# Kernel optimization log

Hardware: AMD Instinct MI355X
Metric: run time of the kernel (lower is better)

The kernel has to match this reference:

```python
import jax, jax.numpy as jnp
import numpy as np

jax.config.update("jax_enable_x64", True)

MANT_SCALE = 8388608.0  # 2**23


def _decode_fp32_bits(bits):
    """[..., 32] {0,1} pulses (MSB-first IEEE-754 float32) -> float64 value."""
    f64 = jnp.float64
    sign = 1.0 - 2.0 * bits[..., 0].astype(f64)
    e = jnp.einsum('...j,j->...', bits[..., 1:9].astype(f64),
                   jnp.exp2(jnp.arange(7, -1, -1, dtype=f64)))
    frac = jnp.einsum('...j,j->...', bits[..., 9:32].astype(f64),
                      jnp.exp2(-jnp.arange(1, 24, dtype=f64)))
    normal = sign * jnp.exp2(e - 127.0) * (1.0 + frac)
    subnorm = sign * jnp.exp2(-126.0) * frac
    return jnp.where(e > 0, normal, subnorm)


def _encode_fp32_bits(y):
    """float64 value already on the fp32 grid -> [..., 32] {0,1} pulses (MSB-first)."""
    f64 = jnp.float64
    sbit = (y < 0).astype(f64)
    a = jnp.abs(y)
    e = jnp.clip(jnp.floor(jnp.log2(jnp.where(a > 0, a, 1.0))), -126.0, 127.0)
    eb = jnp.where(a > 0, e + 127.0, 0.0)          # biased exponent, 0 for zero/subnormal
    frac = jnp.where(eb > 0, a * jnp.exp2(-e) - 1.0, a * jnp.exp2(126.0))
    mant = frac * MANT_SCALE                        # exact integer for fp32-grid y
    ebits = jnp.mod(jnp.floor(eb[..., None] * jnp.exp2(-jnp.arange(7, -1, -1, dtype=f64))), 2.0)
    mbits = jnp.mod(jnp.floor(mant[..., None] * jnp.exp2(-jnp.arange(22, -1, -1, dtype=f64))), 2.0)
    bits = jnp.concatenate([sbit[..., None], ebits, mbits], axis=-1)
    return jnp.where((a > 0)[..., None], bits, 0.0).astype(jnp.float32)


def setup_inputs() -> dict:
    rng = np.random.default_rng(0)
    vals = (rng.standard_normal((1, 2048, 1024)) * 2.0).astype(np.float32)
    words = vals.view(np.uint32)
    shifts = np.arange(31, -1, -1, dtype=np.uint32)
    bits = ((words[..., None] >> shifts) & np.uint32(1)).astype(np.float32)
    return {"x": jnp.asarray(bits)}


def reference(x):
    # GELU(x) ~= x * sigmoid(1.702 * x), all intermediates in fp64 (as the
    # gate-level pipeline does), final result rounded once to fp32 bits.
    xv = _decode_fp32_bits(x)
    y64 = xv * jax.nn.sigmoid(1.702 * xv)
    y32 = y64.astype(jnp.float32).astype(jnp.float64)  # FP64 -> FP32 rounding
    return _encode_fp32_bits(y32)
```

## Files before the change

### kernel.cpp

```cpp
#include <hip/hip_runtime.h>
#include <math.h>


#define LN2C 0x1.62e42fefa39efp-1

typedef unsigned int u32x4 __attribute__((ext_vector_type(4)));

__global__ __launch_bounds__(512, 6) void spike_gelu_kernel(
    const u32x4* __restrict__ in, u32x4* __restrict__ out, int n_vals) {
#pragma clang fp contract(off)
  const double LN2 = LN2C;
  __shared__ double Wdec[8];
  __shared__ double Lms[23];
  __shared__ double E1t[256];
  __shared__ double Vdec[23];
  __shared__ double P2t[254];
  __shared__ uint32_t etab[256];

  const int tid = threadIdx.x;
  const int lane = tid & 63;
  const int wid = tid >> 6;
  const int n_chunks = n_vals * 8;

  const int vwave = blockIdx.x * 512 + wid * 64;
  const int cbase = vwave * 8 + lane;

  u32x4 A[8];
#pragma unroll
  for (int i = 0; i < 8; ++i) {
    int g = cbase + i * 64;
    u32x4 b = {0u, 0u, 0u, 0u};
    if (g < n_chunks) b = __builtin_nontemporal_load(&in[g]);
    A[i] = b;
  }

  if (tid < 8) Wdec[tid] = exp((double)(7 - tid) * LN2);
  if (tid >= 31 && tid < 54) Lms[tid - 31] = exp((double)(31 - tid) * LN2);
  __syncthreads();
  if (tid == 0) {
    E1t[0] = exp(-126.0 * LN2);
  } else if (tid < 256) {
    double e_c = 0.0;
#pragma unroll
    for (int j = 0; j < 8; ++j)
      if ((tid >> (7 - j)) & 1) e_c = e_c + Wdec[j];
    E1t[tid] = exp((e_c - 127.0) * LN2);
  }
  if (tid < 23) Vdec[tid] = exp((double)(-1 - tid) * LN2);
  if (tid < 254) P2t[tid] = exp((double)(126 - tid) * LN2);
  if (tid >= 256) {
    const int tt = tid - 256;
    if (tt >= 1 && tt < 255) {
      double eb = (double)tt;
      uint32_t r = 0;
#pragma unroll
      for (int sc = 7; sc >= 0; --sc) {
        double f = floor(eb * Lms[sc]);
        double md = f - 2.0 * floor(0.5 * f);
        r |= ((uint32_t)md) << (23 + sc);
      }
      etab[tt] = r;
    } else {
      etab[tt] = 0u;
    }
  }
  __syncthreads();

  const int nibshift = 28 - 4 * (lane & 7);
  const int keep = lane & 7;
  uint32_t w0 = 0u;
#pragma unroll
  for (int i = 0; i < 8; ++i) {
    u32x4 b = A[i];
    uint32_t p = (((((b.x >> 23) & 1u) << 3) | (((b.y >> 23) & 1u) << 2) |
                   (((b.z >> 23) & 1u) << 1) | ((b.w >> 23) & 1u)))
                 << nibshift;
    p |= __shfl_xor(p, 1);
    p |= __shfl_xor(p, 2);
    p |= __shfl_xor(p, 4);
    if (keep == i) w0 = p;
  }

  const int v0 = vwave + (lane & 7) * 8 + (lane >> 3);
  const bool ok0 = v0 < n_vals;

  double f0 = 0.0;
#pragma unroll
  for (int j = 0; j < 23; ++j)
    if ((w0 >> (22 - j)) & 1u) f0 = f0 + Vdec[j];
  uint32_t ei0 = (w0 >> 23) & 0xFFu;
  double sg0 = (w0 >> 31) ? -1.0 : 1.0;
  double fa0 = ei0 ? (1.0 + f0) : f0;
  double x0 = (sg0 * E1t[ei0]) * fa0;

  double t0 = 1.702 * x0;
  double e0v = exp(-t0);
  double s0 = 1.0 / (1.0 + e0v);
  double y0 = x0 * s0;
  float yf0 = (float)y0;
  double yd0 = (double)yf0;

  double a0 = fabs(yd0);
  uint32_t yb0 = __float_as_uint(yf0);
  uint32_t Ef0 = (yb0 >> 23) & 0xFFu;
  uint32_t mbf0 = yb0 & 0x7FFFFFu;
  int e00 = (Ef0 == 0u) ? -126 : (int)Ef0 - 127;
  bool pw0 = ok0 && (a0 > 0.0) && (Ef0 != 0u) && (mbf0 == 0u);
  if (__builtin_expect(pw0, 0)) {
    double e0 = floor(log(a0) / LN2);
    e00 = (int)fmin(fmax(e0, -126.0), 127.0);
  }
  double p20 = P2t[e00 + 126];
  double m10 = a0 * p20;
  double mant0 = (m10 - 1.0) * 8388608.0;
  int M0 = (int)rint(mant0);
  uint32_t mb0 = ((uint32_t)M0) & 0x7FFFFFu;
  int T0 = M0 ? __builtin_ctz((uint32_t)M0) : 23;
  int L0 = T0 < 22 ? T0 : 22;
  for (int sc = 0; sc <= L0; ++sc) {
    double f = floor(mant0 * Lms[sc]);
    mb0 = (mb0 & ~(1u << sc)) | (((uint32_t)(((int)f) & 1)) << sc);
  }
  uint32_t ob0 = (yb0 & 0x80000000u) | etab[e00 + 127] | mb0;
  ob0 = (ok0 && a0 > 0.0) ? ob0 : 0u;

  uint32_t wv[8];
#pragma unroll
  for (int i = 0; i < 8; ++i) wv[i] = __shfl(ob0, (lane & 56) + i);
  const int base = 31 - 4 * (lane & 7);
#pragma unroll
  for (int i = 0; i < 8; ++i) {
    int g = cbase + i * 64;
    if (g < n_chunks) {
      uint32_t wa = wv[i];
      u32x4 o;
      o.x = ((wa >> base) & 1u) * 0x3F800000u;
      o.y = ((wa >> (base - 1)) & 1u) * 0x3F800000u;
      o.z = ((wa >> (base - 2)) & 1u) * 0x3F800000u;
      o.w = ((wa >> (base - 3)) & 1u) * 0x3F800000u;
      __builtin_nontemporal_store(o, &out[g]);
    }
  }
}

extern "C" void kernel_launch(void* const* d_in, const int* in_sizes, int n_in,
                              void* d_out, int out_size, void* d_ws, size_t ws_size,
                              hipStream_t stream) {
  int n_vals = in_sizes[0] / 32;
  int grid = (n_vals + 511) / 512;
  spike_gelu_kernel<<<grid, 512, 0, stream>>>(
      (const u32x4*)d_in[0], (u32x4*)d_out, n_vals);
}
```

Measured before the change: 418.9 us.

## Convert to persistent grid-stride kernel with next-tile prefetch

Switches from one 512-thread block per 512 values to 256-thread blocks capped at 1024 and looping over 256-value tiles grid-stride. The next tile's input is loaded into registers before the current tile's compute and store, and the shared lookup tables are built once per block instead of once per tile. This is meant to overlap memory traffic with the fp64 work and amortize the table setup. In exchange the A[] buffer stays live across the compute, raising register pressure, and the fixed grid may underfill the GPU.

```diff
diff --git a/kernel.cpp b/kernel.cpp
--- a/kernel.cpp
+++ b/kernel.cpp
@@ -6,8 +6,9 @@
 
 typedef unsigned int u32x4 __attribute__((ext_vector_type(4)));
 
-__global__ __launch_bounds__(512, 6) void spike_gelu_kernel(
-    const u32x4* __restrict__ in, u32x4* __restrict__ out, int n_vals) {
+__global__ __launch_bounds__(256) void spike_gelu_kernel(
+    const u32x4* __restrict__ in, u32x4* __restrict__ out,
+    int n_vals, int n_tiles) {
 #pragma clang fp contract(off)
   const double LN2 = LN2C;
   __shared__ double Wdec[8];
@@ -21,17 +22,20 @@
   const int lane = tid & 63;
   const int wid = tid >> 6;
   const int n_chunks = n_vals * 8;
+  const int tstep = gridDim.x;
 
-  const int vwave = blockIdx.x * 512 + wid * 64;
-  const int cbase = vwave * 8 + lane;
+  int tile = blockIdx.x;
 
   u32x4 A[8];
+  {
+    const int cb = tile * 2048 + wid * 512 + lane;
 #pragma unroll
-  for (int i = 0; i < 8; ++i) {
-    int g = cbase + i * 64;
-    u32x4 b = {0u, 0u, 0u, 0u};
-    if (g < n_chunks) b = __builtin_nontemporal_load(&in[g]);
-    A[i] = b;
+    for (int i = 0; i < 8; ++i) {
+      int g = cb + i * 64;
+      u32x4 b = {0u, 0u, 0u, 0u};
+      if (g < n_chunks) b = __builtin_nontemporal_load(&in[g]);
+      A[i] = b;
+    }
   }
 
   if (tid < 8) Wdec[tid] = exp((double)(7 - tid) * LN2);
@@ -39,7 +43,7 @@
   __syncthreads();
   if (tid == 0) {
     E1t[0] = exp(-126.0 * LN2);
-  } else if (tid < 256) {
+  } else {
     double e_c = 0.0;
 #pragma unroll
     for (int j = 0; j < 8; ++j)
@@ -48,98 +52,117 @@
   }
   if (tid < 23) Vdec[tid] = exp((double)(-1 - tid) * LN2);
   if (tid < 254) P2t[tid] = exp((double)(126 - tid) * LN2);
-  if (tid >= 256) {
-    const int tt = tid - 256;
-    if (tt >= 1 && tt < 255) {
-      double eb = (double)tt;
-      uint32_t r = 0;
+  if (tid >= 1 && tid < 255) {
+    double eb = (double)tid;
+    uint32_t r = 0;
 #pragma unroll
-      for (int sc = 7; sc >= 0; --sc) {
-        double f = floor(eb * Lms[sc]);
-        double md = f - 2.0 * floor(0.5 * f);
-        r |= ((uint32_t)md) << (23 + sc);
-      }
-      etab[tt] = r;
-    } else {
-      etab[tt] = 0u;
+    for (int sc = 7; sc >= 0; --sc) {
+      double f = floor(eb * Lms[sc]);
+      double md = f - 2.0 * floor(0.5 * f);
+      r |= ((uint32_t)md) << (23 + sc);
     }
+    etab[tid] = r;
+  } else {
+    etab[tid] = 0u;
   }
   __syncthreads();
 
   const int nibshift = 28 - 4 * (lane & 7);
   const int keep = lane & 7;
-  uint32_t w0 = 0u;
+
+  for (;;) {
+    uint32_t w0 = 0u;
 #pragma unroll
-  for (int i = 0; i < 8; ++i) {
-    u32x4 b = A[i];
-    uint32_t p = (((((b.x >> 23) & 1u) << 3) | (((b.y >> 23) & 1u) << 2) |
-                   (((b.z >> 23) & 1u) << 1) | ((b.w >> 23) & 1u)))
-                 << nibshift;
-    p |= __shfl_xor(p, 1);
-    p |= __shfl_xor(p, 2);
-    p |= __shfl_xor(p, 4);
-    if (keep == i) w0 = p;
-  }
+    for (int i = 0; i < 8; ++i) {
+      u32x4 b = A[i];
+      uint32_t p = (((((b.x >> 23) & 1u) << 3) | (((b.y >> 23) & 1u) << 2) |
+                     (((b.z >> 23) & 1u) << 1) | ((b.w >> 23) & 1u)))
+                   << nibshift;
+      p |= __shfl_xor(p, 1);
+      p |= __shfl_xor(p, 2);
+      p |= __shfl_xor(p, 4);
+      if (keep == i) w0 = p;
+    }
+    __builtin_amdgcn_sched_barrier(0);
 
-  const int v0 = vwave + (lane & 7) * 8 + (lane >> 3);
-  const bool ok0 = v0 < n_vals;
+    const int ntile = tile + tstep;
+    const bool havenext = ntile < n_tiles;
+    if (havenext) {
+      const int cb = ntile * 2048 + wid * 512 + lane;
+#pragma unroll
+      for (int i = 0; i < 8; ++i) {
+        int g = cb + i * 64;
+        u32x4 b = {0u, 0u, 0u, 0u};
+        if (g < n_chunks) b = __builtin_nontemporal_load(&in[g]);
+        A[i] = b;
+      }
+    }
 
-  double f0 = 0.0;
+    const int vwave = tile * 256 + wid * 64;
+    const int v0 = vwave + (lane & 7) * 8 + (lane >> 3);
+    const bool ok0 = v0 < n_vals;
+
+    double f0 = 0.0;
 #pragma unroll
-  for (int j = 0; j < 23; ++j)
-    if ((w0 >> (22 - j)) & 1u) f0 = f0 + Vdec[j];
-  uint32_t ei0 = (w0 >> 23) & 0xFFu;
-  double sg0 = (w0 >> 31) ? -1.0 : 1.0;
-  double fa0 = ei0 ? (1.0 + f0) : f0;
-  double x0 = (sg0 * E1t[ei0]) * fa0;
+    for (int j = 0; j < 23; ++j)
+      if ((w0 >> (22 - j)) & 1u) f0 = f0 + Vdec[j];
+    uint32_t ei0 = (w0 >> 23) & 0xFFu;
+    double sg0 = (w0 >> 31) ? -1.0 : 1.0;
+    double fa0 = ei0 ? (1.0 + f0) : f0;
+    double x0 = (sg0 * E1t[ei0]) * fa0;
 
-  double t0 = 1.702 * x0;
-  double e0v = exp(-t0);
-  double s0 = 1.0 / (1.0 + e0v);
-  double y0 = x0 * s0;
-  float yf0 = (float)y0;
-  double yd0 = (double)yf0;
+    double t0 = 1.702 * x0;
+    double e0v = exp(-t0);
+    double s0 = 1.0 / (1.0 + e0v);
+    double y0 = x0 * s0;
+    float yf0 = (float)y0;
+    double yd0 = (double)yf0;
 
-  double a0 = fabs(yd0);
-  uint32_t yb0 = __float_as_uint(yf0);
-  uint32_t Ef0 = (yb0 >> 23) & 0xFFu;
-  uint32_t mbf0 = yb0 & 0x7FFFFFu;
-  int e00 = (Ef0 == 0u) ? -126 : (int)Ef0 - 127;
-  bool pw0 = ok0 && (a0 > 0.0) && (Ef0 != 0u) && (mbf0 == 0u);
-  if (__builtin_expect(pw0, 0)) {
-    double e0 = floor(log(a0) / LN2);
-    e00 = (int)fmin(fmax(e0, -126.0), 127.0);
-  }
-  double p20 = P2t[e00 + 126];
-  double m10 = a0 * p20;
-  double mant0 = (m10 - 1.0) * 8388608.0;
-  int M0 = (int)rint(mant0);
-  uint32_t mb0 = ((uint32_t)M0) & 0x7FFFFFu;
-  int T0 = M0 ? __builtin_ctz((uint32_t)M0) : 23;
-  int L0 = T0 < 22 ? T0 : 22;
-  for (int sc = 0; sc <= L0; ++sc) {
-    double f = floor(mant0 * Lms[sc]);
-    mb0 = (mb0 & ~(1u << sc)) | (((uint32_t)(((int)f) & 1)) << sc);
-  }
-  uint32_t ob0 = (yb0 & 0x80000000u) | etab[e00 + 127] | mb0;
-  ob0 = (ok0 && a0 > 0.0) ? ob0 : 0u;
+    double a0 = fabs(yd0);
+    uint32_t yb0 = __float_as_uint(yf0);
+    uint32_t Ef0 = (yb0 >> 23) & 0xFFu;
+    uint32_t mbf0 = yb0 & 0x7FFFFFu;
+    int e00 = (Ef0 == 0u) ? -126 : (int)Ef0 - 127;
+    bool pw0 = ok0 && (a0 > 0.0) && (Ef0 != 0u) && (mbf0 == 0u);
+    if (__builtin_expect(pw0, 0)) {
+      double e0 = floor(log(a0) / LN2);
+      e00 = (int)fmin(fmax(e0, -126.0), 127.0);
+    }
+    double p20 = P2t[e00 + 126];
+    double m10 = a0 * p20;
+    double mant0 = (m10 - 1.0) * 8388608.0;
+    int M0 = (int)rint(mant0);
+    uint32_t mb0 = ((uint32_t)M0) & 0x7FFFFFu;
+    int T0 = M0 ? __builtin_ctz((uint32_t)M0) : 23;
+    int L0 = T0 < 22 ? T0 : 22;
+    for (int sc = 0; sc <= L0; ++sc) {
+      double f = floor(mant0 * Lms[sc]);
+      mb0 = (mb0 & ~(1u << sc)) | (((uint32_t)(((int)f) & 1)) << sc);
+    }
+    uint32_t ob0 = (yb0 & 0x80000000u) | etab[e00 + 127] | mb0;
+    ob0 = (ok0 && a0 > 0.0) ? ob0 : 0u;
 
-  uint32_t wv[8];
+    uint32_t wv[8];
 #pragma unroll
-  for (int i = 0; i < 8; ++i) wv[i] = __shfl(ob0, (lane & 56) + i);
-  const int base = 31 - 4 * (lane & 7);
+    for (int i = 0; i < 8; ++i) wv[i] = __shfl(ob0, (lane & 56) + i);
+    const int cb = tile * 2048 + wid * 512 + lane;
+    const int base = 31 - 4 * (lane & 7);
 #pragma unroll
-  for (int i = 0; i < 8; ++i) {
-    int g = cbase + i * 64;
-    if (g < n_chunks) {
-      uint32_t wa = wv[i];
-      u32x4 o;
-      o.x = ((wa >> base) & 1u) * 0x3F800000u;
-      o.y = ((wa >> (base - 1)) & 1u) * 0x3F800000u;
-      o.z = ((wa >> (base - 2)) & 1u) * 0x3F800000u;
-      o.w = ((wa >> (base - 3)) & 1u) * 0x3F800000u;
-      __builtin_nontemporal_store(o, &out[g]);
+    for (int i = 0; i < 8; ++i) {
+      int g = cb + i * 64;
+      if (g < n_chunks) {
+        uint32_t wa = wv[i];
+        u32x4 o;
+        o.x = ((wa >> base) & 1u) * 0x3F800000u;
+        o.y = ((wa >> (base - 1)) & 1u) * 0x3F800000u;
+        o.z = ((wa >> (base - 2)) & 1u) * 0x3F800000u;
+        o.w = ((wa >> (base - 3)) & 1u) * 0x3F800000u;
+        __builtin_nontemporal_store(o, &out[g]);
+      }
     }
+
+    if (!havenext) break;
+    tile = ntile;
   }
 }
 
@@ -147,7 +170,8 @@
                               void* d_out, int out_size, void* d_ws, size_t ws_size,
                               hipStream_t stream) {
   int n_vals = in_sizes[0] / 32;
-  int grid = (n_vals + 511) / 512;
-  spike_gelu_kernel<<<grid, 512, 0, stream>>>(
-      (const u32x4*)d_in[0], (u32x4*)d_out, n_vals);
+  int n_tiles = (n_vals + 255) / 256;
+  int grid = n_tiles < 1024 ? n_tiles : 1024;
+  spike_gelu_kernel<<<grid, 256, 0, stream>>>(
+      (const u32x4*)d_in[0], (u32x4*)d_out, n_vals, n_tiles);
 }
```

Measured after the change: 418.2 us. No clear change (-0.2%).
